# Optimization experiments

Measured on AMD Instinct MI355X. Metric: run time of the kernel, lower is better.

The kernel has to match this reference:

```python
import jax, jax.numpy as jnp
import numpy as np

N_NODES = 50000
N_EDGES = 800000
D_IN = 128
D_OUT = 128


def setup_inputs() -> dict:
    key = jax.random.key(0)
    k1, k2, k3, k4, k5 = jax.random.split(key, 5)
    gain = float(np.sqrt(2.0))  # calculate_gain('relu')
    # xavier_uniform bound: gain * sqrt(6/(fan_in+fan_out))
    bound = gain * float(np.sqrt(6.0 / (D_IN + D_OUT)))
    feat = jax.random.normal(k1, (N_NODES, D_IN), dtype=jnp.float32)
    weight = jax.random.uniform(k2, (D_IN, D_OUT), minval=-bound, maxval=bound, dtype=jnp.float32)
    loop_weight = jax.random.uniform(k3, (D_IN, D_OUT), minval=-bound, maxval=bound, dtype=jnp.float32)
    h_bias = jnp.zeros((D_OUT,), dtype=jnp.float32)
    src = jax.random.randint(k4, (N_EDGES,), 0, N_NODES, dtype=jnp.int32)
    dst = jax.random.randint(k5, (N_EDGES,), 0, N_NODES, dtype=jnp.int32)
    return {"feat": feat, "weight": weight, "h_bias": h_bias,
            "loop_weight": loop_weight, "src": src, "dst": dst}


def reference(feat, weight, h_bias, loop_weight, src, dst):
    # message: m_e = feat[src_e] @ W ; aggregate: h_v = sum_{e: dst_e=v} m_e
    # (equivalently transform-then-gather, which avoids the [E, D] matmul)
    transformed = feat @ weight                    # [N, D_out]
    msgs = transformed[src]                        # [E, D_out] gather
    h = jax.ops.segment_sum(msgs, dst, num_segments=feat.shape[0])  # [N, D_out]
    h = h + h_bias                                 # bias
    h = h + feat @ loop_weight                     # self-loop
    # activation=None, dropout=0 -> identity
    return h
```

## Files before the change

### kernel.cpp

```cpp
#include <hip/hip_runtime.h>

#define D 128
#define CAP 64
#define FCHUNK 4096
#define LROW 264

typedef __attribute__((ext_vector_type(8))) short bf16x8;
typedef __attribute__((ext_vector_type(4))) float f32x4;

__device__ inline unsigned short f2bf_rne(float x) {
    unsigned u = __float_as_uint(x);
    return (unsigned short)((u + 0x7FFFu + ((u >> 16) & 1u)) >> 16);
}
__device__ inline float bf_lo(unsigned u) { return __uint_as_float(u << 16); }
__device__ inline float bf_hi(unsigned u) { return __uint_as_float(u & 0xFFFF0000u); }

__global__ __launch_bounds__(256) void prep_kernel(
    const float* __restrict__ W, const float* __restrict__ LW,
    unsigned short* __restrict__ Bt, int* __restrict__ cursor, int ncur)
{
    int tid = blockIdx.x * 256 + threadIdx.x;
    if (tid < 2 * D * D) {
        int n = tid >> 7;
        int k = tid & 127;
        float v = (n < D) ? W[(size_t)k * D + n] : LW[(size_t)k * D + (n - D)];
        Bt[(size_t)n * D + k] = f2bf_rne(v);
    }
    int j = tid - 2 * D * D;
    if (j >= 0 && j < ncur) cursor[j] = 0;
}

__global__ __launch_bounds__(256) void fill_kernel(
    const int* __restrict__ src, const int* __restrict__ dst,
    int* __restrict__ cursor, unsigned short* __restrict__ ebuf,
    int E, int cstride)
{
    const int chunk = blockIdx.x >> 3;
    const int cls   = blockIdx.x & 7;
    const int base  = chunk * FCHUNK;

    for (int i = threadIdx.x; i < FCHUNK; i += 256) {
        const int e = base + i;
        if (e >= E) break;
        const int d = dst[e];
        const int s = src[e];
        if ((d & 7) == cls) {
            int pos = atomicAdd(&cursor[(cls * cstride) + (d >> 3)], 1);
            if (pos < CAP) ebuf[(size_t)d * CAP + pos] = (unsigned short)s;
        }
    }
}

__global__ __launch_bounds__(256) void mfma_transform(
    const float* __restrict__ feat, const unsigned short* __restrict__ Bt,
    unsigned short* __restrict__ T2, int N)
{
    __shared__ unsigned short tile[4 * 16 * LROW];
    const int wave = threadIdx.x >> 6;
    const int lane = threadIdx.x & 63;
    const int wrow0 = blockIdx.x * 64 + wave * 16;
    const int m    = lane & 15;
    const int kg   = lane >> 4;

    int arow_idx = wrow0 + m;
    if (arow_idx >= N) arow_idx = N - 1;
    const float* arow = feat + (size_t)arow_idx * D;

    bf16x8 a[4];
#pragma unroll
    for (int ks = 0; ks < 4; ++ks) {
        const float4 f0 = *(const float4*)(arow + ks * 32 + kg * 8);
        const float4 f1 = *(const float4*)(arow + ks * 32 + kg * 8 + 4);
        bf16x8 v;
        v[0] = (short)f2bf_rne(f0.x); v[1] = (short)f2bf_rne(f0.y);
        v[2] = (short)f2bf_rne(f0.z); v[3] = (short)f2bf_rne(f0.w);
        v[4] = (short)f2bf_rne(f1.x); v[5] = (short)f2bf_rne(f1.y);
        v[6] = (short)f2bf_rne(f1.z); v[7] = (short)f2bf_rne(f1.w);
        a[ks] = v;
    }

    f32x4 acc[16];
#pragma unroll
    for (int t = 0; t < 16; ++t) acc[t] = (f32x4){0.f, 0.f, 0.f, 0.f};

#pragma unroll
    for (int t = 0; t < 16; ++t) {
        const unsigned short* brow = Bt + (size_t)(t * 16 + m) * D;
        bf16x8 b0 = *(const bf16x8*)(brow + 0 * 32 + kg * 8);
        bf16x8 b1 = *(const bf16x8*)(brow + 1 * 32 + kg * 8);
        bf16x8 b2 = *(const bf16x8*)(brow + 2 * 32 + kg * 8);
        bf16x8 b3 = *(const bf16x8*)(brow + 3 * 32 + kg * 8);
        acc[t] = __builtin_amdgcn_mfma_f32_16x16x32_bf16(a[0], b0, acc[t], 0, 0, 0);
        acc[t] = __builtin_amdgcn_mfma_f32_16x16x32_bf16(a[1], b1, acc[t], 0, 0, 0);
        acc[t] = __builtin_amdgcn_mfma_f32_16x16x32_bf16(a[2], b2, acc[t], 0, 0, 0);
        acc[t] = __builtin_amdgcn_mfma_f32_16x16x32_bf16(a[3], b3, acc[t], 0, 0, 0);
    }

    unsigned short* wtile = tile + wave * 16 * LROW;
#pragma unroll
    for (int t = 0; t < 16; ++t) {
#pragma unroll
        for (int r = 0; r < 4; ++r)
            wtile[(kg * 4 + r) * LROW + t * 16 + m] = f2bf_rne(acc[t][r]);
    }
    __syncthreads();

#pragma unroll
    for (int i = 0; i < 8; ++i) {
        const int f   = i * 64 + lane;
        const int row = f >> 5;
        const int cs  = f & 31;
        if (wrow0 + row < N) {
            const uint4 v = *(const uint4*)(wtile + row * LROW + cs * 8);
            *(uint4*)(T2 + (size_t)(wrow0 + row) * 256 + cs * 8) = v;
        }
    }
}

__global__ __launch_bounds__(256) void gather_kernel(
    const unsigned short* __restrict__ ebuf, const int* __restrict__ cursor,
    const unsigned short* __restrict__ T2, const float* __restrict__ bias,
    float* __restrict__ out, int N, int cstride)
{
    const int node = (blockIdx.x * 256 + threadIdx.x) >> 6;
    const int lane = threadIdx.x & 63;
    if (node >= N) return;

    const int h = lane >> 5;
    const int q = lane & 31;

    int deg = cursor[((node & 7) * cstride) + (node >> 3)];
    if (deg > CAP) deg = CAP;

    const unsigned* region = (const unsigned*)(ebuf + (size_t)node * CAP);
    const unsigned short* Tq = T2 + q * 4;

    float a0 = 0.f, a1 = 0.f, a2 = 0.f, a3 = 0.f;

    for (int j = 0; j < deg; j += 16) {
        uint2 u[8];
#pragma unroll
        for (int k = 0; k < 8; ++k) {
            const unsigned w = region[(j >> 1) + k];
            const unsigned s = h ? (w >> 16) : (w & 0xFFFFu);
            u[k] = *(const uint2*)(Tq + (size_t)s * 256);
        }
#pragma unroll
        for (int k = 0; k < 8; ++k) {
            const bool live = (j + 2 * k + h) < deg;
            a0 += live ? bf_lo(u[k].x) : 0.f;
            a1 += live ? bf_hi(u[k].x) : 0.f;
            a2 += live ? bf_lo(u[k].y) : 0.f;
            a3 += live ? bf_hi(u[k].y) : 0.f;
        }
    }

    a0 += __shfl_xor(a0, 32, 64);
    a1 += __shfl_xor(a1, 32, 64);
    a2 += __shfl_xor(a2, 32, 64);
    a3 += __shfl_xor(a3, 32, 64);

    if (h == 0) {
        const uint2 sv = *(const uint2*)(T2 + (size_t)node * 256 + 128 + q * 4);
        const float4 b = *(const float4*)(bias + q * 4);
        float4 o;
        o.x = b.x + bf_lo(sv.x) + a0;
        o.y = b.y + bf_hi(sv.x) + a1;
        o.z = b.z + bf_lo(sv.y) + a2;
        o.w = b.w + bf_hi(sv.y) + a3;
        *(float4*)(out + (size_t)node * D + q * 4) = o;
    }
}

extern "C" void kernel_launch(void* const* d_in, const int* in_sizes, int n_in,
                              void* d_out, int out_size, void* d_ws, size_t ws_size,
                              hipStream_t stream) {
    const float* feat = (const float*)d_in[0];
    const float* W    = (const float*)d_in[1];
    const float* bias = (const float*)d_in[2];
    const float* LW   = (const float*)d_in[3];
    const int*   src  = (const int*)d_in[4];
    const int*   dst  = (const int*)d_in[5];
    float* out = (float*)d_out;

    const int N = in_sizes[0] / D;
    const int E = in_sizes[4];
    const int cstride = (N + 7) >> 3;
    const int ncur = 8 * cstride;

    unsigned short* T2   = (unsigned short*)d_ws;
    unsigned short* Bt   = T2 + (size_t)N * 256;
    unsigned short* ebuf = Bt + 2 * D * D;
    int* cursor = (int*)(ebuf + (size_t)N * CAP);

    {
        const int work = 2 * D * D + ncur;
        prep_kernel<<<dim3((work + 255) / 256), 256, 0, stream>>>(W, LW, Bt, cursor, ncur);
    }

    {
        const int nchunks = (E + FCHUNK - 1) / FCHUNK;
        fill_kernel<<<dim3(nchunks * 8), 256, 0, stream>>>(src, dst, cursor, ebuf, E, cstride);
    }

    mfma_transform<<<dim3((N + 63) / 64), 256, 0, stream>>>(feat, Bt, T2, N);

    gather_kernel<<<dim3((N + 3) / 4), 256, 0, stream>>>(ebuf, cursor, T2, bias, out, N, cstride);
}
```

Measured before the change: 188.8 us.

## Fuse weight prep, edge bucketing and MFMA transform into one kernel

Merges the prep, fill and transform kernels into one launch. The first 256 blocks run a persistent, work-stealing edge bucketing loop that starts on the XCC-matched destination class. The remaining blocks convert W/LW to transposed bf16 in LDS and run the MFMA transform, so fill and transform can overlap and two launches go away. Costs added: every transform block now redundantly converts the full 64 KB of weights into LDS, and the larger LDS footprint may reduce occupancy.

```diff
diff --git a/kernel.cpp b/kernel.cpp
--- a/kernel.cpp
+++ b/kernel.cpp
@@ -3,6 +3,8 @@
 #define D 128
 #define CAP 64
 #define FCHUNK 4096
+#define NB_FILL 256
+#define BTROW 136
 #define LROW 264
 
 typedef __attribute__((ext_vector_type(8))) short bf16x8;
@@ -15,52 +17,68 @@
 __device__ inline float bf_lo(unsigned u) { return __uint_as_float(u << 16); }
 __device__ inline float bf_hi(unsigned u) { return __uint_as_float(u & 0xFFFF0000u); }
 
-__global__ __launch_bounds__(256) void prep_kernel(
-    const float* __restrict__ W, const float* __restrict__ LW,
-    unsigned short* __restrict__ Bt, int* __restrict__ cursor, int ncur)
+__global__ __launch_bounds__(256) void fused_kernel(
+    const float* __restrict__ feat, const float* __restrict__ W,
+    const float* __restrict__ LW,
+    const int* __restrict__ src, const int* __restrict__ dst,
+    int* __restrict__ chunkctr, int* __restrict__ cursor,
+    unsigned short* __restrict__ ebuf, unsigned short* __restrict__ T2,
+    int N, int E, int cstride, int nchunks)
 {
-    int tid = blockIdx.x * 256 + threadIdx.x;
-    if (tid < 2 * D * D) {
-        int n = tid >> 7;
-        int k = tid & 127;
-        float v = (n < D) ? W[(size_t)k * D + n] : LW[(size_t)k * D + (n - D)];
-        Bt[(size_t)n * D + k] = f2bf_rne(v);
-    }
-    int j = tid - 2 * D * D;
-    if (j >= 0 && j < ncur) cursor[j] = 0;
-}
-
-__global__ __launch_bounds__(256) void fill_kernel(
-    const int* __restrict__ src, const int* __restrict__ dst,
-    int* __restrict__ cursor, unsigned short* __restrict__ ebuf,
-    int E, int cstride)
-{
-    const int chunk = blockIdx.x >> 3;
-    const int cls   = blockIdx.x & 7;
-    const int base  = chunk * FCHUNK;
-
-    for (int i = threadIdx.x; i < FCHUNK; i += 256) {
-        const int e = base + i;
-        if (e >= E) break;
-        const int d = dst[e];
-        const int s = src[e];
-        if ((d & 7) == cls) {
-            int pos = atomicAdd(&cursor[(cls * cstride) + (d >> 3)], 1);
-            if (pos < CAP) ebuf[(size_t)d * CAP + pos] = (unsigned short)s;
-        }
-    }
-}
-
-__global__ __launch_bounds__(256) void mfma_transform(
-    const float* __restrict__ feat, const unsigned short* __restrict__ Bt,
-    unsigned short* __restrict__ T2, int N)
-{
-    __shared__ unsigned short tile[4 * 16 * LROW];
-    const int wave = threadIdx.x >> 6;
-    const int lane = threadIdx.x & 63;
-    const int wrow0 = blockIdx.x * 64 + wave * 16;
-    const int m    = lane & 15;
-    const int kg   = lane >> 4;
+    __shared__ unsigned short BtL[256 * BTROW];
+    __shared__ int sh_chunk;
+
+    if ((int)blockIdx.x < NB_FILL) {
+        unsigned xcc;
+        asm volatile("s_getreg_b32 %0, hwreg(HW_REG_XCC_ID)" : "=s"(xcc));
+        xcc &= 7u;
+        const int tid = threadIdx.x;
+
+        for (int off = 0; off < 8; ++off) {
+            const int cls = (int)((xcc + off) & 7u);
+            while (true) {
+                if (tid == 0) sh_chunk = atomicAdd(&chunkctr[cls], 1);
+                __syncthreads();
+                const int c = sh_chunk;
+                __syncthreads();
+                if (c >= nchunks) break;
+                const int base = c * FCHUNK;
+                for (int i = tid; i < FCHUNK; i += 256) {
+                    const int e = base + i;
+                    if (e >= E) break;
+                    const int d = dst[e];
+                    if ((d & 7) == cls) {
+                        int pos = atomicAdd(&cursor[cls * cstride + (d >> 3)], 1);
+                        if (pos < CAP) ebuf[(size_t)d * CAP + pos] = (unsigned short)src[e];
+                    }
+                }
+            }
+        }
+        return;
+    }
+
+    const int mb   = (int)blockIdx.x - NB_FILL;
+    const int row0 = mb * 64;
+
+    for (int i = threadIdx.x; i < 2 * 128 * 32; i += 256) {
+        const int mat = i >> 12;
+        const int r   = i & 4095;
+        const int k   = r >> 5;
+        const int j   = r & 31;
+        const float4 v = ((const float4*)(mat ? LW : W))[k * 32 + j];
+        const int n0 = mat * 128 + j * 4;
+        BtL[(n0 + 0) * BTROW + k] = f2bf_rne(v.x);
+        BtL[(n0 + 1) * BTROW + k] = f2bf_rne(v.y);
+        BtL[(n0 + 2) * BTROW + k] = f2bf_rne(v.z);
+        BtL[(n0 + 3) * BTROW + k] = f2bf_rne(v.w);
+    }
+    __syncthreads();
+
+    const int wave  = threadIdx.x >> 6;
+    const int lane  = threadIdx.x & 63;
+    const int wrow0 = row0 + wave * 16;
+    const int m     = lane & 15;
+    const int kg    = lane >> 4;
 
     int arow_idx = wrow0 + m;
     if (arow_idx >= N) arow_idx = N - 1;
@@ -85,7 +103,7 @@
 
 #pragma unroll
     for (int t = 0; t < 16; ++t) {
-        const unsigned short* brow = Bt + (size_t)(t * 16 + m) * D;
+        const unsigned short* brow = BtL + (t * 16 + m) * BTROW;
         bf16x8 b0 = *(const bf16x8*)(brow + 0 * 32 + kg * 8);
         bf16x8 b1 = *(const bf16x8*)(brow + 1 * 32 + kg * 8);
         bf16x8 b2 = *(const bf16x8*)(brow + 2 * 32 + kg * 8);
@@ -96,6 +114,8 @@
         acc[t] = __builtin_amdgcn_mfma_f32_16x16x32_bf16(a[3], b3, acc[t], 0, 0, 0);
     }
 
+    __syncthreads();
+    unsigned short* tile  = BtL;
     unsigned short* wtile = tile + wave * 16 * LROW;
 #pragma unroll
     for (int t = 0; t < 16; ++t) {
@@ -187,23 +207,20 @@
     const int E = in_sizes[4];
     const int cstride = (N + 7) >> 3;
     const int ncur = 8 * cstride;
+    const int nchunks = (E + FCHUNK - 1) / FCHUNK;
 
     unsigned short* T2   = (unsigned short*)d_ws;
-    unsigned short* Bt   = T2 + (size_t)N * 256;
-    unsigned short* ebuf = Bt + 2 * D * D;
-    int* cursor = (int*)(ebuf + (size_t)N * CAP);
+    unsigned short* ebuf = T2 + (size_t)N * 256;
+    int* chunkctr = (int*)(ebuf + (size_t)N * CAP);
+    int* cursor   = chunkctr + 8;
+
+    hipMemsetAsync(chunkctr, 0, (size_t)(8 + ncur) * sizeof(int), stream);
 
     {
-        const int work = 2 * D * D + ncur;
-        prep_kernel<<<dim3((work + 255) / 256), 256, 0, stream>>>(W, LW, Bt, cursor, ncur);
-    }
-
-    {
-        const int nchunks = (E + FCHUNK - 1) / FCHUNK;
-        fill_kernel<<<dim3(nchunks * 8), 256, 0, stream>>>(src, dst, cursor, ebuf, E, cstride);
-    }
-
-    mfma_transform<<<dim3((N + 63) / 64), 256, 0, stream>>>(feat, Bt, T2, N);
+        const int nb_mfma = (N + 63) / 64;
+        fused_kernel<<<dim3(NB_FILL + nb_mfma), 256, 0, stream>>>(
+            feat, W, LW, src, dst, chunkctr, cursor, ebuf, T2, N, E, cstride, nchunks);
+    }
 
     gather_kernel<<<dim3((N + 3) / 4), 256, 0, stream>>>(ebuf, cursor, T2, bias, out, N, cstride);
 }
```

Result: slower. 227.6 us (+20.5%).
